# Kernel tuning notes

Hardware: AMD Instinct MI355X
Metric: run time of the kernel (lower is better)

Reference implementation:

```python
import jax, jax.numpy as jnp
import numpy as np

E = 8            # num experts
CAP_FACTOR = 1.5
K_THRESH = 0.8
BAL_ALPHA = 0.005
REG_ALPHA = 1e-6
BN_EPS = 1e-5
POOL = 16


def setup_inputs() -> dict:
    key = jax.random.key(0)
    ks = jax.random.split(key, 8)
    B, H, L, D = 128, 1024, 512, 1024
    return {
        "x": jax.random.normal(ks[0], (B, H, L), jnp.float32),
        "conv_w": jax.random.normal(ks[1], (64, H, 3), jnp.float32) / np.float32(np.sqrt(3 * H)),
        "conv_b": jnp.zeros((64,), jnp.float32),
        "bn_gamma": jnp.ones((64 * POOL,), jnp.float32),
        "bn_beta": jnp.zeros((64 * POOL,), jnp.float32),
        "fc1_w": jax.random.normal(ks[2], (128, 64 * POOL), jnp.float32) / np.float32(np.sqrt(64 * POOL)),
        "fc1_b": jnp.zeros((128,), jnp.float32),
        "fc2_w": jax.random.normal(ks[3], (E, 128), jnp.float32) / np.float32(np.sqrt(128)),
        "fc2_b": jnp.zeros((E,), jnp.float32),
        "exp_w": jax.random.normal(ks[4], (E, H, D), jnp.float32) / np.float32(np.sqrt(H)),
        "exp_b": jnp.zeros((E, D), jnp.float32),
    }


def _forward(x, conv_w, conv_b, bn_gamma, bn_beta, fc1_w, fc1_b, fc2_w, fc2_b, exp_w, exp_b):
    B, H, L = x.shape
    # ---- router: Conv1d(H->64,k=3,p=1) -> GELU -> AdaptiveAvgPool1d(16) -> Flatten -> BN -> FC -> GELU -> FC -> softmax
    h = jax.lax.conv_general_dilated(x, conv_w, (1,), ((1, 1),),
                                     dimension_numbers=("NCH", "OIH", "NCH"))
    h = jax.nn.gelu(h + conv_b[None, :, None], approximate=False)          # [B,64,L]; torch GELU is exact erf
    h = h.reshape(B, 64, POOL, L // POOL).mean(-1).reshape(B, 64 * POOL)   # adaptive avg pool (L%16==0) + flatten
    mu, var = h.mean(0), h.var(0)                                          # training-mode (Sync)BatchNorm: batch stats
    h = (h - mu) / jnp.sqrt(var + BN_EPS) * bn_gamma + bn_beta
    h = jax.nn.gelu(h @ fc1_w.T + fc1_b, approximate=False)
    rw = jax.nn.softmax(h @ fc2_w.T + fc2_b, axis=1)                       # [B,E]; expert dropout = identity (eval)
    # ---- dynamic k: smallest k s.t. cumsum of sorted probs > threshold; only max over batch is used
    topk_w, topk_idx = jax.lax.top_k(rw, E)                                # full descending sort
    cum = jnp.cumsum(topk_w, axis=1)
    over = cum > K_THRESH
    k_per = jnp.where(jnp.any(over, axis=1), jnp.argmax(over, axis=1) + 1, E)
    max_k = jnp.max(jnp.clip(k_per, 1, E))
    col_valid = jnp.arange(E)[None, :] < max_k                             # broadcast [B,E]; cols >= max_k unused
    assign = jnp.where(col_valid, topk_idx, -1)
    # ---- capacity enforcement: per expert keep the `capacity` highest-weight assignments, drop the rest (-1)
    capacity = max(1, int(B * CAP_FACTOR / E))
    flat_idx, flat_w = assign.reshape(-1), topk_w.reshape(-1)              # row-major [B*E], matches torch flatten

    def keep_for_expert(e):
        m = flat_idx == e
        order = jnp.argsort(-jnp.where(m, flat_w, -jnp.inf))               # descending within expert e
        ranks = jnp.zeros_like(order).at[order].set(jnp.arange(order.shape[0]))
        return m & (ranks < capacity)

    keep = jax.vmap(keep_for_expert)(jnp.arange(E))                        # [E, B*E]
    counts = keep.sum(axis=1).astype(jnp.float32)                          # == bincount of valid final indices
    final_idx = jnp.where(jnp.any(keep, axis=0), flat_idx, -1).reshape(B, E)
    # ---- experts: mean-pool over length, per-expert Linear(H->D); gather each sample's selected experts
    pooled = x.mean(axis=2)                                                # [B,H]
    y = jnp.einsum("bh,ehd->bed", pooled, exp_w) + exp_b[None]             # [B,E,D] all-expert outputs
    outputs = jnp.take_along_axis(y, jnp.clip(final_idx, 0)[..., None], axis=1)
    outputs = jnp.where(final_idx[..., None] >= 0, outputs, 0.0)           # dropped slots contribute zeros
    # ---- combine: softmax over the max_k slots; dropped (-1) slots enter softmax with logit 0, as in torch
    logits = jnp.where(col_valid, topk_w * (final_idx >= 0), -jnp.inf)
    norm_w = jax.nn.softmax(logits, axis=1)                                # [B,E]
    pooler = jnp.einsum("bkd,bk->bd", outputs, norm_w)                     # [B,D]
    # ---- losses / stats
    usage = rw.mean(0)
    reg = jnp.sum(exp_w * exp_w) + jnp.sum(exp_b * exp_b)                  # sum ||param||_2^2 over expert params
    added_loss = BAL_ALPHA * jnp.var(usage, ddof=1) + REG_ALPHA * reg      # torch.var is unbiased
    return pooler, added_loss, usage, counts


def reference(x, conv_w, conv_b, bn_gamma, bn_beta, fc1_w, fc1_b, fc2_w, fc2_b, exp_w, exp_b):
    return _forward(x, conv_w, conv_b, bn_gamma, bn_beta, fc1_w, fc1_b, fc2_w, fc2_b, exp_w, exp_b)
```

## Files before the change

kernel.cpp:

```cpp
#include <hip/hip_runtime.h>
#include <hip/hip_bf16.h>
#include <math.h>

#define NB 128
#define NH 1024
#define NL 512
#define OC 64
#define NE 8
#define ND 1024
#define CAPACITY 24

static const size_t WS_PART  = 0;
static const size_t WS_WSEP  = 1048576;
static const size_t WS_PXT   = 2097152;
static const size_t WS_HPOOL = 2228224;
static const size_t WS_SCALE = 2359296;
static const size_t WS_SHIFT = 2360320;
static const size_t WS_TKW   = 2377728;
static const size_t WS_TKI   = 2378752;
static const size_t WS_USAGE = 2379784;
static const size_t WS_VARU  = 2379792;
static const size_t WS_REG   = 2379793;
static const size_t WS_CNT   = 2379794;
static const size_t WS_WMAT  = 2380832;
static const size_t WS_RW    = 2381856;
static const size_t WS_KP    = 2382880;

typedef __attribute__((ext_vector_type(8))) short bf16x8;
typedef __attribute__((ext_vector_type(4))) float f32x4;

__device__ __forceinline__ float gelu_exact(float v) {
    return 0.5f * v * (1.0f + erff(v * 0.70710678118654752440f));
}

__device__ __forceinline__ unsigned short f2bf_rne(float f) {
    unsigned int u = __float_as_uint(f);
    unsigned int r = u + 0x7FFFu + ((u >> 16) & 1u);
    return (unsigned short)(r >> 16);
}
__device__ __forceinline__ float bf2f(unsigned short h) {
    return __uint_as_float(((unsigned int)h) << 16);
}

__device__ __forceinline__ unsigned cvtpk_bf16(float a, float b) {
    unsigned r;
    asm("v_cvt_pk_bf16_f32 %0, %1, %2" : "=v"(r) : "v"(a), "v"(b));
    return r;
}

__global__ __launch_bounds__(256) void k_wsplit(const float* __restrict__ cw, float* __restrict__ ws)
{
    if (blockIdx.x == 0 && threadIdx.x == 0) ws[WS_REG] = 0.0f;
    unsigned short* wsep = (unsigned short*)(ws + WS_WSEP);
    int i = blockIdx.x * 256 + threadIdx.x;
    int lane = i & 63;
    int split = (i >> 6) & 1;
    int mt = (i >> 7) & 3;
    int rest = i >> 9;
    int j = rest % 3;
    int it = rest / 3;
    int o = mt * 16 + (lane & 15);
    int hb = it * 32 + ((lane >> 4) << 3);
    unsigned short v8[8];
#pragma unroll
    for (int e = 0; e < 8; ++e) {
        float v = cw[((size_t)o * 1024 + hb + e) * 3 + j];
        unsigned short hi = f2bf_rne(v);
        v8[e] = split ? f2bf_rne(v - bf2f(hi)) : hi;
    }
    *(uint4*)(wsep + ((size_t)((it * 3 + j) * 4 + mt) * 2 + split) * 512 + lane * 8) = *(uint4*)v8;
}

__device__ __forceinline__ void cvt_unit(unsigned int* X, int lq, int h4,
                                         const float4* v, float* sh)
{
    sh[0] = sh[1] = sh[2] = sh[3] = 0.f;
#pragma unroll
    for (int i = 0; i < 4; ++i) {
        float a0 = ((const float*)&v[0])[i];
        float a1 = ((const float*)&v[1])[i];
        float a2 = ((const float*)&v[2])[i];
        float a3 = ((const float*)&v[3])[i];
        sh[0] += a0; sh[1] += a1; sh[2] += a2; sh[3] += a3;
        unsigned h01 = cvtpk_bf16(a0, a1);
        unsigned h23 = cvtpk_bf16(a2, a3);
        float r0 = a0 - __uint_as_float(h01 << 16);
        float r1 = a1 - __uint_as_float(h01 & 0xFFFF0000u);
        float r2 = a2 - __uint_as_float(h23 << 16);
        float r3 = a3 - __uint_as_float(h23 & 0xFFFF0000u);
        unsigned l01 = cvtpk_bf16(r0, r1);
        unsigned l23 = cvtpk_bf16(r2, r3);
        int r = lq * 4 + i;
        unsigned int* dst = X + r * 34 + ((2 * h4) ^ ((r & 3) << 2));
        *(uint2*)dst = make_uint2(h01, h23);
        *(uint2*)(dst + 16) = make_uint2(l01, l23);
    }
}

__global__ __launch_bounds__(256, 2) void k_convmfma(const float* __restrict__ x,
                                                     const float* __restrict__ cb,
                                                     float* __restrict__ ws)
{
    __shared__ unsigned int Xb[2][136 * 34];
    __shared__ float xs2[3][128];
    __shared__ float scb[64];

    const int lc = blockIdx.x, b = blockIdx.y;
    const int l0 = lc * 128;
    const int tid = threadIdx.x;
    const int wv = tid >> 6, lane = tid & 63;
    const int h4 = tid & 7;
    const int lqi = 1 + (tid >> 3);
    const bool has_halo = (tid < 16);
    const int lqh = (tid < 8) ? 0 : 33;
    const bool halo_ok = (tid < 8) ? (lc > 0) : (lc < 3);

    const unsigned short* wsg = (const unsigned short*)(ws + WS_WSEP);
    const float* xbase = x + (size_t)b * (NH * NL);
    float* poolp = ws + WS_PART + ((size_t)(lc * 128 + b)) * 1024;

    if (tid < 64) scb[tid] = cb[tid];

    f32x4 acc[4][2];
#pragma unroll
    for (int mt = 0; mt < 4; ++mt)
#pragma unroll
        for (int nt = 0; nt < 2; ++nt) acc[mt][nt] = (f32x4){0.f, 0.f, 0.f, 0.f};

    float4 xA[4], hA[4], xB[4], hB[4];

    auto xload = [&](int itL, float4* xc, float4* hc) {
        const int hn = itL * 32;
        const float* p = xbase + (size_t)(hn + h4 * 4) * NL + (l0 - 4 + lqi * 4);
#pragma unroll
        for (int jj = 0; jj < 4; ++jj) xc[jj] = *(const float4*)(p + jj * NL);
        if (has_halo) {
            int gl = l0 - 4 + lqh * 4;
#pragma unroll
            for (int jj = 0; jj < 4; ++jj)
                hc[jj] = halo_ok ? *(const float4*)(xbase + (size_t)(hn + h4 * 4 + jj) * NL + gl)
                                 : make_float4(0.f, 0.f, 0.f, 0.f);
        }
    };

    auto body = [&](int it, float4* xc, float4* hc) {
        unsigned int* Xw = Xb[it & 1];
        bf16x8 Ar[3][4][2];
        {
            const unsigned short* abase = wsg + (size_t)it * 12288 + lane * 8;
#pragma unroll
            for (int j = 0; j < 3; ++j)
#pragma unroll
                for (int mt = 0; mt < 4; ++mt) {
                    Ar[j][mt][0] = *(const bf16x8*)(abase + (size_t)((j * 8 + mt * 2) * 512));
                    Ar[j][mt][1] = *(const bf16x8*)(abase + (size_t)((j * 8 + mt * 2 + 1) * 512));
                }
        }
        {
            float sh[4];
            cvt_unit(Xw, lqi, h4, xc, sh);
#pragma unroll
            for (int jj = 0; jj < 4; ++jj) {
                float s = sh[jj];
                s += __shfl_xor(s, 8, 64);
                s += __shfl_xor(s, 16, 64);
                s += __shfl_xor(s, 32, 64);
                if ((lane >> 3) == 0) xs2[it % 3][wv * 32 + h4 * 4 + jj] = s;
            }
            if (has_halo) { float d[4]; cvt_unit(Xw, lqh, h4, hc, d); }
        }
        __syncthreads();
        if (it > 0 && tid < 32) {
            const float* S = xs2[(it - 1) % 3];
            poolp[(it - 1) * 32 + tid] = S[tid] + S[32 + tid] + S[64 + tid] + S[96 + tid];
        }
        if (it < 30) xload(it + 2, xc, hc);
        const int g4 = (lane >> 4) << 2;
#pragma unroll
        for (int j = 0; j < 3; ++j) {
            bf16x8 Bh[2], Bl[2];
#pragma unroll
            for (int nt = 0; nt < 2; ++nt) {
                int rx = 3 + j + wv * 32 + nt * 16 + (lane & 15);
                const unsigned int* bp = Xw + rx * 34 + (g4 ^ ((rx & 3) << 2));
                Bh[nt] = *(const bf16x8*)bp;
                Bl[nt] = *(const bf16x8*)(bp + 16);
            }
#pragma unroll
            for (int mt = 0; mt < 4; ++mt)
#pragma unroll
                for (int nt = 0; nt < 2; ++nt) {
                    acc[mt][nt] = __builtin_amdgcn_mfma_f32_16x16x32_bf16(Ar[j][mt][0], Bh[nt], acc[mt][nt], 0, 0, 0);
                    acc[mt][nt] = __builtin_amdgcn_mfma_f32_16x16x32_bf16(Ar[j][mt][0], Bl[nt], acc[mt][nt], 0, 0, 0);
                    acc[mt][nt] = __builtin_amdgcn_mfma_f32_16x16x32_bf16(Ar[j][mt][1], Bh[nt], acc[mt][nt], 0, 0, 0);
                }
        }
    };

    xload(0, xA, hA);
    xload(1, xB, hB);

    for (int it2 = 0; it2 < 32; it2 += 2) {
        body(it2, xA, hA);
        body(it2 + 1, xB, hB);
    }
    if (tid < 32) {
        const float* S = xs2[31 % 3];
        poolp[31 * 32 + tid] = S[tid] + S[32 + tid] + S[64 + tid] + S[96 + tid];
    }

    {
        const int g = lane >> 4, cidx = lane & 15;
#pragma unroll
        for (int mt = 0; mt < 4; ++mt) {
            float s[4];
#pragma unroll
            for (int r = 0; r < 4; ++r) {
                int o = mt * 16 + g * 4 + r;
                float bo = scb[o];
                s[r] = gelu_exact(acc[mt][0][r] + bo) + gelu_exact(acc[mt][1][r] + bo);
            }
#pragma unroll
            for (int m = 1; m < 16; m <<= 1) {
#pragma unroll
                for (int r = 0; r < 4; ++r) s[r] += __shfl_xor(s[r], m, 64);
            }
            if (cidx == 0) {
#pragma unroll
                for (int r = 0; r < 4; ++r) {
                    int o = mt * 16 + g * 4 + r;
                    ws[WS_HPOOL + (size_t)b * 1024 + o * 16 + lc * 4 + wv] = s[r] * (1.0f / 32.0f);
                }
            }
        }
    }
}

__global__ __launch_bounds__(256) void k_mid(const float* __restrict__ g,
                                             const float* __restrict__ bet,
                                             float* __restrict__ ws)
{
    int bx = blockIdx.x;
    if (bx < 512) {
        int id = bx * 256 + threadIdx.x;
        int b = id >> 10, h = id & 1023;
        float s = 0.0f;
#pragma unroll
        for (int lcc = 0; lcc < 4; lcc++) s += ws[WS_PART + ((size_t)(lcc * 128 + b)) * 1024 + h];
        ws[WS_PXT + (size_t)h * 128 + b] = s * (1.0f / 512.0f);
    } else {
        int f = (bx - 512) * 256 + threadIdx.x;
        const float* hp = ws + WS_HPOOL;
        float s = 0.0f;
        for (int b = 0; b < 128; b++) s += hp[(size_t)b * 1024 + f];
        float mu = s * (1.0f / 128.0f);
        float v = 0.0f;
        for (int b = 0; b < 128; b++) { float d = hp[(size_t)b * 1024 + f] - mu; v += d * d; }
        float var = v * (1.0f / 128.0f);
        float sc = g[f] / sqrtf(var + 1e-5f);
        ws[WS_SCALE + f] = sc;
        ws[WS_SHIFT + f] = bet[f] - mu * sc;
    }
}

__global__ __launch_bounds__(256) void k_fused(const float* __restrict__ w1,
                                               const float* __restrict__ b1,
                                               const float* __restrict__ w2,
                                               const float* __restrict__ b2,
                                               const float* __restrict__ ew,
                                               const float* __restrict__ eb,
                                               float* __restrict__ ws)
{
    __shared__ float smem[5376];
    const int bx = blockIdx.x;
    const int tid = threadIdx.x;

    if (bx < 512) {
        float* a_s = smem;
        float* b_s = smem + 4096;
        float* red2 = smem + 5120;
        const int e = bx >> 6, dt = (bx >> 1) & 31, ks = bx & 1;
        const int tb = tid >> 3, td = tid & 7;
        float acc[4][4];
#pragma unroll
        for (int i = 0; i < 4; i++)
#pragma unroll
            for (int j = 0; j < 4; j++) acc[i][j] = 0.0f;
        float ssq = 0.0f;

        const float* pxt = ws + WS_PXT;
        for (int kt = 0; kt < 512; kt += 32) {
            __syncthreads();
            for (int idx = tid; idx < 4096; idx += 256) {
                int kk = idx >> 7, bb = idx & 127;
                a_s[kk * 128 + bb] = pxt[(size_t)(ks * 512 + kt + kk) * 128 + bb];
            }
            for (int idx = tid; idx < 1024; idx += 256) {
                int kk = idx >> 5, d = idx & 31;
                float v = ew[(size_t)e * 1048576 + (size_t)(ks * 512 + kt + kk) * 1024 + dt * 32 + d];
                b_s[kk * 32 + d] = v;
                ssq += v * v;
            }
            __syncthreads();
#pragma unroll 4
            for (int kk = 0; kk < 32; kk++) {
                float4 av = *(const float4*)&a_s[kk * 128 + tb * 4];
                float4 bv = *(const float4*)&b_s[kk * 32 + td * 4];
                float aa[4] = {av.x, av.y, av.z, av.w};
                float bb4[4] = {bv.x, bv.y, bv.z, bv.w};
#pragma unroll
                for (int i = 0; i < 4; i++)
#pragma unroll
                    for (int j = 0; j < 4; j++) acc[i][j] = fmaf(aa[i], bb4[j], acc[i][j]);
            }
        }
        float* outp = ws + WS_PART + ((size_t)(ks * 8 + e) * 128) * 1024 + dt * 32;
#pragma unroll
        for (int i = 0; i < 4; i++) {
            int bb = tb * 4 + i;
            *(float4*)(outp + (size_t)bb * 1024 + td * 4) =
                make_float4(acc[i][0], acc[i][1], acc[i][2], acc[i][3]);
        }
        if (bx == 0)
            for (int i = tid; i < 8192; i += 256) { float v = eb[i]; ssq += v * v; }
        red2[tid] = ssq;
        __syncthreads();
        for (int off = 128; off > 0; off >>= 1) {
            if (tid < off) red2[tid] += red2[tid + off];
            __syncthreads();
        }
        if (tid == 0) atomicAdd(ws + WS_REG, red2[0]);
    } else {
        float* hb  = smem;
        float* red = smem + 1024;
        float* ha  = smem + 1280;
        float* w2s = smem + 1408;
        float* lg  = smem + 2432;
        const int b = bx - 512;
        const float* hp = ws + WS_HPOOL + (size_t)b * 1024;
        for (int k = tid; k < 1024; k += 256)
            hb[k] = hp[k] * ws[WS_SCALE + k] + ws[WS_SHIFT + k];
        for (int i = tid; i < 1024; i += 256) w2s[i] = w2[i];
        __syncthreads();
        int o = tid & 127, kh = tid >> 7;
        const float4* wrp = (const float4*)(w1 + (size_t)o * 1024 + kh * 512);
        const float* hx = hb + kh * 512;
        float acc = 0.0f;
#pragma unroll 4
        for (int k = 0; k < 128; k++) {
            float4 w = wrp[k];
            acc = fmaf(hx[4 * k], w.x, acc);     acc = fmaf(hx[4 * k + 1], w.y, acc);
            acc = fmaf(hx[4 * k + 2], w.z, acc); acc = fmaf(hx[4 * k + 3], w.w, acc);
        }
        red[tid] = acc;
        __syncthreads();
        if (tid < 128)
            ha[tid] = gelu_exact(red[tid] + red[tid + 128] + b1[tid]);
        __syncthreads();
        if (tid < 8) {
            float a2 = b2[tid];
            for (int k = 0; k < 128; k++) a2 = fmaf(ha[k], w2s[tid * 128 + k], a2);
            lg[tid] = a2;
        }
        __syncthreads();
        if (tid == 0) {
            float rw[8];
            float m = -1e30f;
#pragma unroll
            for (int e = 0; e < 8; e++) m = fmaxf(m, lg[e]);
            float s = 0.0f;
#pragma unroll
            for (int e = 0; e < 8; e++) { rw[e] = expf(lg[e] - m); s += rw[e]; }
            float inv = 1.0f / s;
#pragma unroll
            for (int e = 0; e < 8; e++) { rw[e] *= inv; ws[WS_RW + b * 8 + e] = rw[e]; }
            float tw[8]; int ti[8]; unsigned used = 0;
#pragma unroll
            for (int r = 0; r < 8; r++) {
                float bv = -1e30f; int bi = 0;
#pragma unroll
                for (int e = 0; e < 8; e++) {
                    bool take = !((used >> e) & 1u) && (rw[e] > bv);
                    bv = take ? rw[e] : bv;
                    bi = take ? e : bi;
                }
                used |= (1u << bi);
                tw[r] = bv; ti[r] = bi;
            }
            float cum = 0.0f; int kp = 8;
#pragma unroll
            for (int r = 0; r < 8; r++) {
                cum += tw[r];
                if (cum > 0.8f) { kp = r + 1; break; }
            }
#pragma unroll
            for (int r = 0; r < 8; r++) {
                ws[WS_TKW + b * 8 + r] = tw[r];
                ((int*)ws)[WS_TKI + b * 8 + r] = ti[r];
            }
            ((int*)ws)[WS_KP + b] = kp;
        }
    }
}

__global__ __launch_bounds__(128) void k_route(float* __restrict__ ws)
{
    __shared__ float tkw_s[1024];
    __shared__ int   tki_s[1024];
    __shared__ int   keep_s[1024];
    __shared__ float wv_s[128];
    __shared__ int   sv_s[128];
    __shared__ float usg[8];
    __shared__ int   cnt_s[8];
    __shared__ int   mk;

    const int tid = threadIdx.x;
    const int b = tid;
    if (tid == 0) mk = 0;
    if (tid < 8) cnt_s[tid] = 0;
    __syncthreads();
    atomicMax(&mk, ((const int*)ws)[WS_KP + b]);
#pragma unroll
    for (int r = 0; r < 8; r++) {
        tkw_s[b * 8 + r] = ws[WS_TKW + b * 8 + r];
        tki_s[b * 8 + r] = ((const int*)ws)[WS_TKI + b * 8 + r];
    }
    __syncthreads();
    const int maxk = mk;

    if (tid < 8) {
        float s2 = 0.0f;
        for (int bb = 0; bb < 128; bb++) s2 += ws[WS_RW + bb * 8 + tid];
        float u = s2 * (1.0f / 128.0f);
        usg[tid] = u;
        ws[WS_USAGE + tid] = u;
    }
    __syncthreads();
    if (tid == 0) {
        float mu = 0.0f;
#pragma unroll
        for (int e = 0; e < 8; e++) mu += usg[e];
        mu *= (1.0f / 8.0f);
        float v = 0.0f;
#pragma unroll
        for (int e = 0; e < 8; e++) { float d = usg[e] - mu; v += d * d; }
        ws[WS_VARU] = v * (1.0f / 7.0f);
    }

    for (int e = 0; e < 8; ++e) {
        float myw = 0.0f; int mys = -1;
        for (int k = 0; k < maxk; k++)
            if (tki_s[b * 8 + k] == e) { myw = tkw_s[b * 8 + k]; mys = b * 8 + k; }
        wv_s[b] = myw; sv_s[b] = mys;
        __syncthreads();
        if (mys >= 0) {
            int rank = 0;
            for (int b2 = 0; b2 < 128; b2++) {
                int s2 = sv_s[b2];
                if (s2 >= 0) {
                    float w2v = wv_s[b2];
                    if (w2v > myw || (w2v == myw && s2 < mys)) rank++;
                }
            }
            int kept = (rank < CAPACITY) ? 1 : 0;
            keep_s[mys] = kept;
            if (kept) atomicAdd(&cnt_s[e], 1);
        }
        __syncthreads();
    }
    if (tid < 8) ws[WS_CNT + tid] = (float)cnt_s[tid];

    float lv[8]; int kept[8]; int idx[8];
#pragma unroll
    for (int k = 0; k < 8; k++) {
        if (k < maxk) {
            kept[k] = keep_s[b * 8 + k];
            idx[k] = tki_s[b * 8 + k];
            lv[k] = kept[k] ? tkw_s[b * 8 + k] : 0.0f;
        } else { kept[k] = 0; idx[k] = -1; lv[k] = -1e30f; }
    }
    float mx = -1e30f;
#pragma unroll
    for (int k = 0; k < 8; k++) if (k < maxk) mx = fmaxf(mx, lv[k]);
    float s3 = 0.0f; float ev[8];
#pragma unroll
    for (int k = 0; k < 8; k++) { ev[k] = (k < maxk) ? expf(lv[k] - mx) : 0.0f; s3 += ev[k]; }
    float inv3 = 1.0f / s3;
    float Wr[8] = {0, 0, 0, 0, 0, 0, 0, 0};
#pragma unroll
    for (int k = 0; k < 8; k++) {
        if (kept[k]) {
            float v = ev[k] * inv3;
#pragma unroll
            for (int e = 0; e < 8; e++) Wr[e] += (idx[k] == e) ? v : 0.0f;
        }
    }
#pragma unroll
    for (int e = 0; e < 8; e++) ws[WS_WMAT + b * 8 + e] = Wr[e];
}

__global__ __launch_bounds__(256) void k_final(const float* __restrict__ eb,
                                               const float* __restrict__ ws,
                                               float* __restrict__ out)
{
    int id = blockIdx.x * 256 + threadIdx.x;
    int b = id >> 8, dq = id & 255;
    const float* wm = ws + WS_WMAT + b * 8;
    const float* Y = ws + WS_PART;
    float4 s = make_float4(0.f, 0.f, 0.f, 0.f);
#pragma unroll
    for (int e = 0; e < 8; e++) {
        float4 y0 = *(const float4*)(Y + ((size_t)e * 128 + b) * 1024 + dq * 4);
        float4 y1 = *(const float4*)(Y + ((size_t)(8 + e) * 128 + b) * 1024 + dq * 4);
        float4 bb = *(const float4*)(eb + (size_t)e * 1024 + dq * 4);
        float w = wm[e];
        s.x += w * (y0.x + y1.x + bb.x);
        s.y += w * (y0.y + y1.y + bb.y);
        s.z += w * (y0.z + y1.z + bb.z);
        s.w += w * (y0.w + y1.w + bb.w);
    }
    *(float4*)(out + (size_t)b * 1024 + dq * 4) = s;
    if (blockIdx.x == 0) {
        int t = threadIdx.x;
        if (t == 0) out[131072] = 0.005f * ws[WS_VARU] + 1e-6f * ws[WS_REG];
        else if (t >= 1 && t < 9)  out[131072 + t] = ws[WS_USAGE + t - 1];
        else if (t >= 9 && t < 17) out[131072 + t] = ws[WS_CNT + t - 9];
    }
}

extern "C" void kernel_launch(void* const* d_in, const int* in_sizes, int n_in,
                              void* d_out, int out_size, void* d_ws, size_t ws_size,
                              hipStream_t stream)
{
    const float* x   = (const float*)d_in[0];
    const float* cw  = (const float*)d_in[1];
    const float* cb  = (const float*)d_in[2];
    const float* bng = (const float*)d_in[3];
    const float* bnb = (const float*)d_in[4];
    const float* f1w = (const float*)d_in[5];
    const float* f1b = (const float*)d_in[6];
    const float* f2w = (const float*)d_in[7];
    const float* f2b = (const float*)d_in[8];
    const float* ew  = (const float*)d_in[9];
    const float* eb  = (const float*)d_in[10];
    float* ws  = (float*)d_ws;
    float* out = (float*)d_out;

    k_wsplit  <<<192, 256, 0, stream>>>(cw, ws);
    k_convmfma<<<dim3(4, 128), 256, 0, stream>>>(x, cb, ws);
    k_mid     <<<516, 256, 0, stream>>>(bng, bnb, ws);
    k_fused   <<<640, 256, 0, stream>>>(f1w, f1b, f2w, f2b, ew, eb, ws);
    k_route   <<<1, 128, 0, stream>>>(ws);
    k_final   <<<128, 256, 0, stream>>>(eb, ws, out);
}
```

Before: 312.0 us.

## Split conv reduction over channels across two blocks with a combine kernel

The conv MFMA kernel is templated to split the 1024-channel reduction into two halves along a new grid z dimension. This doubles the block count from 512 to 1024 to improve occupancy across the CUs. Each half writes raw accumulators to workspace, and a new k_conv2 kernel sums them and applies bias, GELU and pooling. The split adds about 8 MB of partial-accumulator traffic plus an extra launch, and it falls back to the unsplit path when the workspace is too small.

```diff
diff --git a/kernel.cpp b/kernel.cpp
--- a/kernel.cpp
+++ b/kernel.cpp
@@ -25,6 +25,8 @@
 static const size_t WS_WMAT  = 2380832;
 static const size_t WS_RW    = 2381856;
 static const size_t WS_KP    = 2382880;
+static const size_t WS_CP    = 2400000;
+static const size_t WS_END   = WS_CP + 2ull * 4 * 128 * 8192;
 
 typedef __attribute__((ext_vector_type(8))) short bf16x8;
 typedef __attribute__((ext_vector_type(4))) float f32x4;
@@ -97,6 +99,7 @@
     }
 }
 
+template<int SPLIT>
 __global__ __launch_bounds__(256, 2) void k_convmfma(const float* __restrict__ x,
                                                      const float* __restrict__ cb,
                                                      float* __restrict__ ws)
@@ -105,7 +108,9 @@
     __shared__ float xs2[3][128];
     __shared__ float scb[64];
 
+    const int NIT = 32 / SPLIT;
     const int lc = blockIdx.x, b = blockIdx.y;
+    const int kh = (SPLIT == 2) ? blockIdx.z : 0;
     const int l0 = lc * 128;
     const int tid = threadIdx.x;
     const int wv = tid >> 6, lane = tid & 63;
@@ -117,9 +122,9 @@
 
     const unsigned short* wsg = (const unsigned short*)(ws + WS_WSEP);
     const float* xbase = x + (size_t)b * (NH * NL);
-    float* poolp = ws + WS_PART + ((size_t)(lc * 128 + b)) * 1024;
-
-    if (tid < 64) scb[tid] = cb[tid];
+    float* poolp = ws + WS_PART + ((size_t)(lc * 128 + b)) * 1024 + (size_t)kh * NIT * 32;
+
+    if (SPLIT == 1 && tid < 64) scb[tid] = cb[tid];
 
     f32x4 acc[4][2];
 #pragma unroll
@@ -130,7 +135,7 @@
     float4 xA[4], hA[4], xB[4], hB[4];
 
     auto xload = [&](int itL, float4* xc, float4* hc) {
-        const int hn = itL * 32;
+        const int hn = (kh * NIT + itL) * 32;
         const float* p = xbase + (size_t)(hn + h4 * 4) * NL + (l0 - 4 + lqi * 4);
 #pragma unroll
         for (int jj = 0; jj < 4; ++jj) xc[jj] = *(const float4*)(p + jj * NL);
@@ -147,7 +152,7 @@
         unsigned int* Xw = Xb[it & 1];
         bf16x8 Ar[3][4][2];
         {
-            const unsigned short* abase = wsg + (size_t)it * 12288 + lane * 8;
+            const unsigned short* abase = wsg + (size_t)(kh * NIT + it) * 12288 + lane * 8;
 #pragma unroll
             for (int j = 0; j < 3; ++j)
 #pragma unroll
@@ -174,7 +179,7 @@
             const float* S = xs2[(it - 1) % 3];
             poolp[(it - 1) * 32 + tid] = S[tid] + S[32 + tid] + S[64 + tid] + S[96 + tid];
         }
-        if (it < 30) xload(it + 2, xc, hc);
+        if (it < NIT - 2) xload(it + 2, xc, hc);
         const int g4 = (lane >> 4) << 2;
 #pragma unroll
         for (int j = 0; j < 3; ++j) {
@@ -200,16 +205,23 @@
     xload(0, xA, hA);
     xload(1, xB, hB);
 
-    for (int it2 = 0; it2 < 32; it2 += 2) {
+    for (int it2 = 0; it2 < NIT; it2 += 2) {
         body(it2, xA, hA);
         body(it2 + 1, xB, hB);
     }
     if (tid < 32) {
-        const float* S = xs2[31 % 3];
-        poolp[31 * 32 + tid] = S[tid] + S[32 + tid] + S[64 + tid] + S[96 + tid];
-    }
-
-    {
+        const float* S = xs2[(NIT - 1) % 3];
+        poolp[(NIT - 1) * 32 + tid] = S[tid] + S[32 + tid] + S[64 + tid] + S[96 + tid];
+    }
+
+    if (SPLIT == 2) {
+        float* cp = ws + WS_CP + (((size_t)(kh * 4 + lc) * 128 + b) * 2048 + tid * 8) * 4;
+#pragma unroll
+        for (int mt = 0; mt < 4; ++mt)
+#pragma unroll
+            for (int nt = 0; nt < 2; ++nt)
+                *(f32x4*)(cp + (mt * 2 + nt) * 4) = acc[mt][nt];
+    } else {
         const int g = lane >> 4, cidx = lane & 15;
 #pragma unroll
         for (int mt = 0; mt < 4; ++mt) {
@@ -231,6 +243,53 @@
                     int o = mt * 16 + g * 4 + r;
                     ws[WS_HPOOL + (size_t)b * 1024 + o * 16 + lc * 4 + wv] = s[r] * (1.0f / 32.0f);
                 }
+            }
+        }
+    }
+}
+
+__global__ __launch_bounds__(256) void k_conv2(const float* __restrict__ cb,
+                                               float* __restrict__ ws)
+{
+    __shared__ float scb[64];
+    const int lc = blockIdx.x, b = blockIdx.y;
+    const int tid = threadIdx.x;
+    const int wv = tid >> 6, lane = tid & 63;
+    if (tid < 64) scb[tid] = cb[tid];
+    __syncthreads();
+
+    const float* cp0 = ws + WS_CP + (((size_t)(0 * 4 + lc) * 128 + b) * 2048 + tid * 8) * 4;
+    const float* cp1 = ws + WS_CP + (((size_t)(1 * 4 + lc) * 128 + b) * 2048 + tid * 8) * 4;
+    f32x4 acc[4][2];
+#pragma unroll
+    for (int mt = 0; mt < 4; ++mt)
+#pragma unroll
+        for (int nt = 0; nt < 2; ++nt) {
+            f32x4 a0 = *(const f32x4*)(cp0 + (mt * 2 + nt) * 4);
+            f32x4 a1 = *(const f32x4*)(cp1 + (mt * 2 + nt) * 4);
+            acc[mt][nt] = a0 + a1;
+        }
+
+    const int g = lane >> 4, cidx = lane & 15;
+#pragma unroll
+    for (int mt = 0; mt < 4; ++mt) {
+        float s[4];
+#pragma unroll
+        for (int r = 0; r < 4; ++r) {
+            int o = mt * 16 + g * 4 + r;
+            float bo = scb[o];
+            s[r] = gelu_exact(acc[mt][0][r] + bo) + gelu_exact(acc[mt][1][r] + bo);
+        }
+#pragma unroll
+        for (int m = 1; m < 16; m <<= 1) {
+#pragma unroll
+            for (int r = 0; r < 4; ++r) s[r] += __shfl_xor(s[r], m, 64);
+        }
+        if (cidx == 0) {
+#pragma unroll
+            for (int r = 0; r < 4; ++r) {
+                int o = mt * 16 + g * 4 + r;
+                ws[WS_HPOOL + (size_t)b * 1024 + o * 16 + lc * 4 + wv] = s[r] * (1.0f / 32.0f);
             }
         }
     }
@@ -546,10 +605,17 @@
     float* ws  = (float*)d_ws;
     float* out = (float*)d_out;
 
-    k_wsplit  <<<192, 256, 0, stream>>>(cw, ws);
-    k_convmfma<<<dim3(4, 128), 256, 0, stream>>>(x, cb, ws);
-    k_mid     <<<516, 256, 0, stream>>>(bng, bnb, ws);
-    k_fused   <<<640, 256, 0, stream>>>(f1w, f1b, f2w, f2b, ew, eb, ws);
-    k_route   <<<1, 128, 0, stream>>>(ws);
-    k_final   <<<128, 256, 0, stream>>>(eb, ws, out);
-}
+    const bool split_ok = ws_size >= (size_t)WS_END * sizeof(float);
+
+    k_wsplit<<<192, 256, 0, stream>>>(cw, ws);
+    if (split_ok) {
+        k_convmfma<2><<<dim3(4, 128, 2), 256, 0, stream>>>(x, cb, ws);
+        k_conv2<<<dim3(4, 128), 256, 0, stream>>>(cb, ws);
+    } else {
+        k_convmfma<1><<<dim3(4, 128), 256, 0, stream>>>(x, cb, ws);
+    }
+    k_mid  <<<516, 256, 0, stream>>>(bng, bnb, ws);
+    k_fused<<<640, 256, 0, stream>>>(f1w, f1b, f2w, f2b, ew, eb, ws);
+    k_route<<<1, 128, 0, stream>>>(ws);
+    k_final<<<128, 256, 0, stream>>>(eb, ws, out);
+}
```

Result: slower. 325.9 us (+4.5%).

## Fuse mid reduction and routing into neighbouring kernels to cut launches

Applied to the files above, without the earlier changes.

Removes the k_mid kernel. The partial-sum reduction and transpose of the pooled input now happen inside the expert GEMM tile loads, reading the conv partials directly into padded shared memory. Each router block recomputes the BatchNorm batch statistics redundantly, and k_route is folded into k_final, so every block redoes the capacity ranking before combining its own row. This saves two launches and the intermediate workspace round trips. In exchange it adds redundant work per block: 128 router blocks each scan all of HPOOL, the GEMM A-tile loads are strided, and 128 final blocks repeat the serial ranking loop.

```diff
diff --git a/kernel.cpp b/kernel.cpp
--- a/kernel.cpp
+++ b/kernel.cpp
@@ -12,19 +12,13 @@
 
 static const size_t WS_PART  = 0;
 static const size_t WS_WSEP  = 1048576;
-static const size_t WS_PXT   = 2097152;
 static const size_t WS_HPOOL = 2228224;
-static const size_t WS_SCALE = 2359296;
-static const size_t WS_SHIFT = 2360320;
 static const size_t WS_TKW   = 2377728;
 static const size_t WS_TKI   = 2378752;
-static const size_t WS_USAGE = 2379784;
-static const size_t WS_VARU  = 2379792;
 static const size_t WS_REG   = 2379793;
-static const size_t WS_CNT   = 2379794;
-static const size_t WS_WMAT  = 2380832;
 static const size_t WS_RW    = 2381856;
 static const size_t WS_KP    = 2382880;
+static const size_t WS_Y     = 2400000;
 
 typedef __attribute__((ext_vector_type(8))) short bf16x8;
 typedef __attribute__((ext_vector_type(4))) float f32x4;
@@ -236,49 +230,24 @@
     }
 }
 
-__global__ __launch_bounds__(256) void k_mid(const float* __restrict__ g,
-                                             const float* __restrict__ bet,
-                                             float* __restrict__ ws)
-{
-    int bx = blockIdx.x;
-    if (bx < 512) {
-        int id = bx * 256 + threadIdx.x;
-        int b = id >> 10, h = id & 1023;
-        float s = 0.0f;
-#pragma unroll
-        for (int lcc = 0; lcc < 4; lcc++) s += ws[WS_PART + ((size_t)(lcc * 128 + b)) * 1024 + h];
-        ws[WS_PXT + (size_t)h * 128 + b] = s * (1.0f / 512.0f);
-    } else {
-        int f = (bx - 512) * 256 + threadIdx.x;
-        const float* hp = ws + WS_HPOOL;
-        float s = 0.0f;
-        for (int b = 0; b < 128; b++) s += hp[(size_t)b * 1024 + f];
-        float mu = s * (1.0f / 128.0f);
-        float v = 0.0f;
-        for (int b = 0; b < 128; b++) { float d = hp[(size_t)b * 1024 + f] - mu; v += d * d; }
-        float var = v * (1.0f / 128.0f);
-        float sc = g[f] / sqrtf(var + 1e-5f);
-        ws[WS_SCALE + f] = sc;
-        ws[WS_SHIFT + f] = bet[f] - mu * sc;
-    }
-}
-
 __global__ __launch_bounds__(256) void k_fused(const float* __restrict__ w1,
                                                const float* __restrict__ b1,
                                                const float* __restrict__ w2,
                                                const float* __restrict__ b2,
                                                const float* __restrict__ ew,
                                                const float* __restrict__ eb,
+                                               const float* __restrict__ bng,
+                                               const float* __restrict__ bnb,
                                                float* __restrict__ ws)
 {
-    __shared__ float smem[5376];
+    __shared__ float smem[5504];
     const int bx = blockIdx.x;
     const int tid = threadIdx.x;
 
     if (bx < 512) {
         float* a_s = smem;
-        float* b_s = smem + 4096;
-        float* red2 = smem + 5120;
+        float* b_s = smem + 4224;
+        float* red2 = smem + 5248;
         const int e = bx >> 6, dt = (bx >> 1) & 31, ks = bx & 1;
         const int tb = tid >> 3, td = tid & 7;
         float acc[4][4];
@@ -288,12 +257,17 @@
             for (int j = 0; j < 4; j++) acc[i][j] = 0.0f;
         float ssq = 0.0f;
 
-        const float* pxt = ws + WS_PXT;
+        const float* P = ws + WS_PART;
         for (int kt = 0; kt < 512; kt += 32) {
             __syncthreads();
             for (int idx = tid; idx < 4096; idx += 256) {
-                int kk = idx >> 7, bb = idx & 127;
-                a_s[kk * 128 + bb] = pxt[(size_t)(ks * 512 + kt + kk) * 128 + bb];
+                int bb = idx >> 5, hh = idx & 31;
+                size_t hoff = (size_t)(ks * 512 + kt + hh);
+                float s = P[((size_t)(0 * 128 + bb)) * 1024 + hoff];
+                s += P[((size_t)(1 * 128 + bb)) * 1024 + hoff];
+                s += P[((size_t)(2 * 128 + bb)) * 1024 + hoff];
+                s += P[((size_t)(3 * 128 + bb)) * 1024 + hoff];
+                a_s[hh * 132 + bb] = s * (1.0f / 512.0f);
             }
             for (int idx = tid; idx < 1024; idx += 256) {
                 int kk = idx >> 5, d = idx & 31;
@@ -304,7 +278,7 @@
             __syncthreads();
 #pragma unroll 4
             for (int kk = 0; kk < 32; kk++) {
-                float4 av = *(const float4*)&a_s[kk * 128 + tb * 4];
+                float4 av = *(const float4*)&a_s[kk * 132 + tb * 4];
                 float4 bv = *(const float4*)&b_s[kk * 32 + td * 4];
                 float aa[4] = {av.x, av.y, av.z, av.w};
                 float bb4[4] = {bv.x, bv.y, bv.z, bv.w};
@@ -314,7 +288,7 @@
                     for (int j = 0; j < 4; j++) acc[i][j] = fmaf(aa[i], bb4[j], acc[i][j]);
             }
         }
-        float* outp = ws + WS_PART + ((size_t)(ks * 8 + e) * 128) * 1024 + dt * 32;
+        float* outp = ws + WS_Y + ((size_t)(ks * 8 + e) * 128) * 1024 + dt * 32;
 #pragma unroll
         for (int i = 0; i < 4; i++) {
             int bb = tb * 4 + i;
@@ -331,16 +305,49 @@
         }
         if (tid == 0) atomicAdd(ws + WS_REG, red2[0]);
     } else {
-        float* hb  = smem;
-        float* red = smem + 1024;
-        float* ha  = smem + 1280;
-        float* w2s = smem + 1408;
-        float* lg  = smem + 2432;
+        float* hb   = smem;
+        float* red  = smem + 1024;
+        float* ha   = smem + 1280;
+        float* w2s  = smem + 1408;
+        float* lg   = smem + 2432;
+        float* sc_s = smem + 2440;
+        float* sh_s = smem + 3464;
         const int b = bx - 512;
+
+        {
+            const float* hpa = ws + WS_HPOOL;
+            int f0 = tid * 4;
+            float s0 = 0.f, s1 = 0.f, s2 = 0.f, s3 = 0.f;
+            for (int b2 = 0; b2 < 128; ++b2) {
+                float4 v = *(const float4*)(hpa + (size_t)b2 * 1024 + f0);
+                s0 += v.x; s1 += v.y; s2 += v.z; s3 += v.w;
+            }
+            float mu0 = s0 * (1.0f / 128.0f), mu1 = s1 * (1.0f / 128.0f);
+            float mu2 = s2 * (1.0f / 128.0f), mu3 = s3 * (1.0f / 128.0f);
+            float v0 = 0.f, v1 = 0.f, v2 = 0.f, v3 = 0.f;
+            for (int b2 = 0; b2 < 128; ++b2) {
+                float4 v = *(const float4*)(hpa + (size_t)b2 * 1024 + f0);
+                float d0 = v.x - mu0, d1 = v.y - mu1, d2 = v.z - mu2, d3 = v.w - mu3;
+                v0 += d0 * d0; v1 += d1 * d1; v2 += d2 * d2; v3 += d3 * d3;
+            }
+            float4 g4 = *(const float4*)(bng + f0);
+            float4 be4 = *(const float4*)(bnb + f0);
+            float sc0 = g4.x / sqrtf(v0 * (1.0f / 128.0f) + 1e-5f);
+            float sc1 = g4.y / sqrtf(v1 * (1.0f / 128.0f) + 1e-5f);
+            float sc2 = g4.z / sqrtf(v2 * (1.0f / 128.0f) + 1e-5f);
+            float sc3 = g4.w / sqrtf(v3 * (1.0f / 128.0f) + 1e-5f);
+            sc_s[f0] = sc0; sc_s[f0 + 1] = sc1; sc_s[f0 + 2] = sc2; sc_s[f0 + 3] = sc3;
+            sh_s[f0] = be4.x - mu0 * sc0;
+            sh_s[f0 + 1] = be4.y - mu1 * sc1;
+            sh_s[f0 + 2] = be4.z - mu2 * sc2;
+            sh_s[f0 + 3] = be4.w - mu3 * sc3;
+        }
+        for (int i = tid; i < 1024; i += 256) w2s[i] = w2[i];
+        __syncthreads();
+
         const float* hp = ws + WS_HPOOL + (size_t)b * 1024;
         for (int k = tid; k < 1024; k += 256)
-            hb[k] = hp[k] * ws[WS_SCALE + k] + ws[WS_SHIFT + k];
-        for (int i = tid; i < 1024; i += 256) w2s[i] = w2[i];
+            hb[k] = hp[k] * sc_s[k] + sh_s[k];
         __syncthreads();
         int o = tid & 127, kh = tid >> 7;
         const float4* wrp = (const float4*)(w1 + (size_t)o * 1024 + kh * 512);
@@ -403,7 +410,9 @@
     }
 }
 
-__global__ __launch_bounds__(128) void k_route(float* __restrict__ ws)
+__global__ __launch_bounds__(256) void k_final(const float* __restrict__ eb,
+                                               const float* __restrict__ ws,
+                                               float* __restrict__ out)
 {
     __shared__ float tkw_s[1024];
     __shared__ int   tki_s[1024];
@@ -413,47 +422,31 @@
     __shared__ float usg[8];
     __shared__ int   cnt_s[8];
     __shared__ int   mk;
-
+    __shared__ float wmat_s[8];
+    __shared__ float vu_s;
+
+    const int bx = blockIdx.x;
     const int tid = threadIdx.x;
-    const int b = tid;
     if (tid == 0) mk = 0;
     if (tid < 8) cnt_s[tid] = 0;
+    for (int i = tid; i < 1024; i += 256) {
+        tkw_s[i] = ws[WS_TKW + i];
+        tki_s[i] = ((const int*)ws)[WS_TKI + i];
+    }
     __syncthreads();
-    atomicMax(&mk, ((const int*)ws)[WS_KP + b]);
-#pragma unroll
-    for (int r = 0; r < 8; r++) {
-        tkw_s[b * 8 + r] = ws[WS_TKW + b * 8 + r];
-        tki_s[b * 8 + r] = ((const int*)ws)[WS_TKI + b * 8 + r];
-    }
+    if (tid < 128) atomicMax(&mk, ((const int*)ws)[WS_KP + tid]);
     __syncthreads();
     const int maxk = mk;
 
-    if (tid < 8) {
-        float s2 = 0.0f;
-        for (int bb = 0; bb < 128; bb++) s2 += ws[WS_RW + bb * 8 + tid];
-        float u = s2 * (1.0f / 128.0f);
-        usg[tid] = u;
-        ws[WS_USAGE + tid] = u;
-    }
-    __syncthreads();
-    if (tid == 0) {
-        float mu = 0.0f;
-#pragma unroll
-        for (int e = 0; e < 8; e++) mu += usg[e];
-        mu *= (1.0f / 8.0f);
-        float v = 0.0f;
-#pragma unroll
-        for (int e = 0; e < 8; e++) { float d = usg[e] - mu; v += d * d; }
-        ws[WS_VARU] = v * (1.0f / 7.0f);
-    }
-
     for (int e = 0; e < 8; ++e) {
         float myw = 0.0f; int mys = -1;
-        for (int k = 0; k < maxk; k++)
-            if (tki_s[b * 8 + k] == e) { myw = tkw_s[b * 8 + k]; mys = b * 8 + k; }
-        wv_s[b] = myw; sv_s[b] = mys;
-        __syncthreads();
-        if (mys >= 0) {
+        if (tid < 128) {
+            for (int k = 0; k < maxk; k++)
+                if (tki_s[tid * 8 + k] == e) { myw = tkw_s[tid * 8 + k]; mys = tid * 8 + k; }
+            wv_s[tid] = myw; sv_s[tid] = mys;
+        }
+        __syncthreads();
+        if (tid < 128 && mys >= 0) {
             int rank = 0;
             for (int b2 = 0; b2 < 128; b2++) {
                 int s2 = sv_s[b2];
@@ -468,63 +461,74 @@
         }
         __syncthreads();
     }
-    if (tid < 8) ws[WS_CNT + tid] = (float)cnt_s[tid];
-
-    float lv[8]; int kept[8]; int idx[8];
-#pragma unroll
-    for (int k = 0; k < 8; k++) {
-        if (k < maxk) {
-            kept[k] = keep_s[b * 8 + k];
-            idx[k] = tki_s[b * 8 + k];
-            lv[k] = kept[k] ? tkw_s[b * 8 + k] : 0.0f;
-        } else { kept[k] = 0; idx[k] = -1; lv[k] = -1e30f; }
-    }
-    float mx = -1e30f;
-#pragma unroll
-    for (int k = 0; k < 8; k++) if (k < maxk) mx = fmaxf(mx, lv[k]);
-    float s3 = 0.0f; float ev[8];
-#pragma unroll
-    for (int k = 0; k < 8; k++) { ev[k] = (k < maxk) ? expf(lv[k] - mx) : 0.0f; s3 += ev[k]; }
-    float inv3 = 1.0f / s3;
-    float Wr[8] = {0, 0, 0, 0, 0, 0, 0, 0};
-#pragma unroll
-    for (int k = 0; k < 8; k++) {
-        if (kept[k]) {
-            float v = ev[k] * inv3;
-#pragma unroll
-            for (int e = 0; e < 8; e++) Wr[e] += (idx[k] == e) ? v : 0.0f;
-        }
-    }
-#pragma unroll
-    for (int e = 0; e < 8; e++) ws[WS_WMAT + b * 8 + e] = Wr[e];
-}
-
-__global__ __launch_bounds__(256) void k_final(const float* __restrict__ eb,
-                                               const float* __restrict__ ws,
-                                               float* __restrict__ out)
-{
-    int id = blockIdx.x * 256 + threadIdx.x;
-    int b = id >> 8, dq = id & 255;
-    const float* wm = ws + WS_WMAT + b * 8;
-    const float* Y = ws + WS_PART;
-    float4 s = make_float4(0.f, 0.f, 0.f, 0.f);
-#pragma unroll
-    for (int e = 0; e < 8; e++) {
-        float4 y0 = *(const float4*)(Y + ((size_t)e * 128 + b) * 1024 + dq * 4);
-        float4 y1 = *(const float4*)(Y + ((size_t)(8 + e) * 128 + b) * 1024 + dq * 4);
-        float4 bb = *(const float4*)(eb + (size_t)e * 1024 + dq * 4);
-        float w = wm[e];
-        s.x += w * (y0.x + y1.x + bb.x);
-        s.y += w * (y0.y + y1.y + bb.y);
-        s.z += w * (y0.z + y1.z + bb.z);
-        s.w += w * (y0.w + y1.w + bb.w);
-    }
-    *(float4*)(out + (size_t)b * 1024 + dq * 4) = s;
-    if (blockIdx.x == 0) {
-        int t = threadIdx.x;
-        if (t == 0) out[131072] = 0.005f * ws[WS_VARU] + 1e-6f * ws[WS_REG];
-        else if (t >= 1 && t < 9)  out[131072 + t] = ws[WS_USAGE + t - 1];
-        else if (t >= 9 && t < 17) out[131072 + t] = ws[WS_CNT + t - 9];
+
+    if (tid < 8) {
+        float s2 = 0.0f;
+        for (int bb = 0; bb < 128; bb++) s2 += ws[WS_RW + bb * 8 + tid];
+        usg[tid] = s2 * (1.0f / 128.0f);
+    }
+    __syncthreads();
+    if (tid == 0) {
+        float lv[8]; int kept[8]; int idx[8];
+#pragma unroll
+        for (int k = 0; k < 8; k++) {
+            if (k < maxk) {
+                kept[k] = keep_s[bx * 8 + k];
+                idx[k] = tki_s[bx * 8 + k];
+                lv[k] = kept[k] ? tkw_s[bx * 8 + k] : 0.0f;
+            } else { kept[k] = 0; idx[k] = -1; lv[k] = -1e30f; }
+        }
+        float mx = -1e30f;
+#pragma unroll
+        for (int k = 0; k < 8; k++) if (k < maxk) mx = fmaxf(mx, lv[k]);
+        float s3 = 0.0f; float ev[8];
+#pragma unroll
+        for (int k = 0; k < 8; k++) { ev[k] = (k < maxk) ? expf(lv[k] - mx) : 0.0f; s3 += ev[k]; }
+        float inv3 = 1.0f / s3;
+        float Wr[8] = {0, 0, 0, 0, 0, 0, 0, 0};
+#pragma unroll
+        for (int k = 0; k < 8; k++) {
+            if (kept[k]) {
+                float v = ev[k] * inv3;
+#pragma unroll
+                for (int e = 0; e < 8; e++) Wr[e] += (idx[k] == e) ? v : 0.0f;
+            }
+        }
+#pragma unroll
+        for (int e = 0; e < 8; e++) wmat_s[e] = Wr[e];
+        float mu = 0.0f;
+#pragma unroll
+        for (int e = 0; e < 8; e++) mu += usg[e];
+        mu *= (1.0f / 8.0f);
+        float v = 0.0f;
+#pragma unroll
+        for (int e = 0; e < 8; e++) { float d = usg[e] - mu; v += d * d; }
+        vu_s = v * (1.0f / 7.0f);
+    }
+    __syncthreads();
+
+    {
+        const int dq = tid;
+        const float* Y = ws + WS_Y;
+        float4 s = make_float4(0.f, 0.f, 0.f, 0.f);
+#pragma unroll
+        for (int e = 0; e < 8; e++) {
+            float4 y0 = *(const float4*)(Y + ((size_t)e * 128 + bx) * 1024 + dq * 4);
+            float4 y1 = *(const float4*)(Y + ((size_t)(8 + e) * 128 + bx) * 1024 + dq * 4);
+            float4 bb = *(const float4*)(eb + (size_t)e * 1024 + dq * 4);
+            float w = wmat_s[e];
+            s.x += w * (y0.x + y1.x + bb.x);
+            s.y += w * (y0.y + y1.y + bb.y);
+            s.z += w * (y0.z + y1.z + bb.z);
+            s.w += w * (y0.w + y1.w + bb.w);
+        }
+        *(float4*)(out + (size_t)bx * 1024 + dq * 4) = s;
+    }
+    if (bx == 0) {
+        int t = tid;
+        if (t == 0) out[131072] = 0.005f * vu_s + 1e-6f * ws[WS_REG];
+        else if (t >= 1 && t < 9)  out[131072 + t] = usg[t - 1];
+        else if (t >= 9 && t < 17) out[131072 + t] = (float)cnt_s[t - 9];
     }
 }
 
@@ -548,8 +552,6 @@
 
     k_wsplit  <<<192, 256, 0, stream>>>(cw, ws);
     k_convmfma<<<dim3(4, 128), 256, 0, stream>>>(x, cb, ws);
-    k_mid     <<<516, 256, 0, stream>>>(bng, bnb, ws);
-    k_fused   <<<640, 256, 0, stream>>>(f1w, f1b, f2w, f2b, ew, eb, ws);
-    k_route   <<<1, 128, 0, stream>>>(ws);
+    k_fused   <<<640, 256, 0, stream>>>(f1w, f1b, f2w, f2b, ew, eb, bng, bnb, ws);
     k_final   <<<128, 256, 0, stream>>>(eb, ws, out);
 }
```

After: 299.4 us. 1.04x faster.
